# Kernel tuning notes

Hardware: AMD Instinct MI355X
Metric: run time of the kernel (lower is better)

The kernel has to match this reference:

```python
import jax, jax.numpy as jnp
import numpy as np

TEMPERATURE = 0.5
EPS = 1e-12  # matches torch F.normalize default eps


def setup_inputs() -> dict:
    key = jax.random.key(0)
    k1, k2 = jax.random.split(key)
    B, D = 4096, 1024
    emb_i = jax.random.normal(k1, (B, D), dtype=jnp.float32)
    emb_j = jax.random.normal(k2, (B, D), dtype=jnp.float32)
    return {"emb_i": emb_i, "emb_j": emb_j}


def _l2_normalize(x):
    # torch F.normalize(dim=1): x / max(||x||, eps)
    n = jnp.sqrt(jnp.sum(x * x, axis=1, keepdims=True))
    return x / jnp.maximum(n, EPS)


def reference(emb_i, emb_j):
    B = emb_i.shape[0]
    z_i = _l2_normalize(emb_i)
    z_j = _l2_normalize(emb_j)
    z = jnp.concatenate([z_i, z_j], axis=0)  # [2B, D]
    # cosine similarity of unit vectors == dot product -> single GEMM
    sim = jnp.einsum('nd,md->nm', z, z)  # [2B, 2B]
    sim_ij = jnp.diagonal(sim, offset=B)   # [B]
    sim_ji = jnp.diagonal(sim, offset=-B)  # [B]
    positives = jnp.concatenate([sim_ij, sim_ji], axis=0)  # [2B]
    nominator = jnp.exp(positives / TEMPERATURE)
    neg_mask = 1.0 - jnp.eye(2 * B, dtype=sim.dtype)
    denominator = jnp.sum(neg_mask * jnp.exp(sim / TEMPERATURE), axis=1)  # [2B]
    loss_partial = -jnp.log(nominator / denominator)
    return jnp.sum(loss_partial) / (2 * B)
```

## Files before the change

### kernel.cpp

```cpp
#include <hip/hip_runtime.h>
#include <hip/hip_bf16.h>
#include <math.h>

#define B_ROWS 4096
#define N_ROWS 8192
#define D_DIM  1024
#define NTILES 64
#define NSLOT  64
#define NPAIRS (NTILES * (NTILES + 1) / 2)
#define NXCD 8

#define BM 128
#define BK 64
#define NT (D_DIM / BK)
#define SLOT_BYTES 16384
#define RING 2

typedef __attribute__((ext_vector_type(4))) int i32x4;

__device__ __forceinline__ void load_lds_16B(const void* g, void* l) {
  __builtin_amdgcn_global_load_lds(
      (const __attribute__((address_space(1))) void*)g,
      (__attribute__((address_space(3))) void*)l, 16, 0, 0);
}

#define VMCNT0() asm volatile("s_waitcnt vmcnt(0)" ::: "memory")
#define LGKM0()  asm volatile("s_waitcnt lgkmcnt(0)" ::: "memory")
#define BARRIER() asm volatile("s_barrier" ::: "memory")

__global__ __launch_bounds__(256) void normalize_kernel(
    const float* __restrict__ emb_i, const float* __restrict__ emb_j,
    char* __restrict__ zq, float* __restrict__ rowS) {
  const int lane = threadIdx.x & 63;
  const int wave = threadIdx.x >> 6;
  const int row = blockIdx.x * 4 + wave;
  const float* src = (row < B_ROWS) ? (emb_i + (size_t)row * D_DIM)
                                    : (emb_j + (size_t)(row - B_ROWS) * D_DIM);
  const float4* s4 = reinterpret_cast<const float4*>(src);
  float4 v0 = s4[lane], v1 = s4[lane + 64], v2 = s4[lane + 128],
         v3 = s4[lane + 192];

  float ss = v0.x * v0.x + v0.y * v0.y + v0.z * v0.z + v0.w * v0.w +
             v1.x * v1.x + v1.y * v1.y + v1.z * v1.z + v1.w * v1.w +
             v2.x * v2.x + v2.y * v2.y + v2.z * v2.z + v2.w * v2.w +
             v3.x * v3.x + v3.y * v3.y + v3.z * v3.z + v3.w * v3.w;
#pragma unroll
  for (int m = 32; m; m >>= 1) ss += __shfl_xor(ss, m, 64);
  const float scale = 1.0f / fmaxf(sqrtf(ss), 1e-12f);

  float z[16];
  z[0] = v0.x * scale;  z[1] = v0.y * scale;  z[2] = v0.z * scale;
  z[3] = v0.w * scale;  z[4] = v1.x * scale;  z[5] = v1.y * scale;
  z[6] = v1.z * scale;  z[7] = v1.w * scale;  z[8] = v2.x * scale;
  z[9] = v2.y * scale;  z[10] = v2.z * scale; z[11] = v2.w * scale;
  z[12] = v3.x * scale; z[13] = v3.y * scale; z[14] = v3.z * scale;
  z[15] = v3.w * scale;

  float am = 0.0f;
#pragma unroll
  for (int i = 0; i < 16; ++i) am = fmaxf(am, fabsf(z[i]));
#pragma unroll
  for (int m = 32; m; m >>= 1) am = fmaxf(am, __shfl_xor(am, m, 64));
  const float s = am * (1.0f / 127.0f);
  const float inv = (am > 0.0f) ? 127.0f / am : 0.0f;

  char4* dst = reinterpret_cast<char4*>(zq + (size_t)row * D_DIM);
#pragma unroll
  for (int i = 0; i < 4; ++i) {
    char4 pk;
    pk.x = (char)(int)rintf(z[i * 4 + 0] * inv);
    pk.y = (char)(int)rintf(z[i * 4 + 1] * inv);
    pk.z = (char)(int)rintf(z[i * 4 + 2] * inv);
    pk.w = (char)(int)rintf(z[i * 4 + 3] * inv);
    dst[lane + 64 * i] = pk;
  }
  if (lane == 0) rowS[row] = s;
}

__global__ __launch_bounds__(256, 4) void simexp_kernel(
    const char* __restrict__ zq, const float* __restrict__ rowS,
    float* __restrict__ partial, float* __restrict__ dn,
    float* __restrict__ pos) {
  __shared__ __align__(16) char ldsbuf[RING * SLOT_BYTES];
  __shared__ float rowAcc[BM];
  __shared__ float colAcc[BM];
  __shared__ float sRow[BM];
  __shared__ float sCol[BM];

  const int tid = threadIdx.x;

  const int work = (blockIdx.x % NXCD) * (NPAIRS / NXCD) + blockIdx.x / NXCD;

  int rem = work;
  int ti = 0;
  while (rem >= NTILES - ti) {
    rem -= NTILES - ti;
    ++ti;
  }
  const int tj = ti + rem;
  const bool diag = (ti == tj);
  const int row0 = ti * BM;
  const int m0 = tj * BM;

  if (tid < BM) {
    rowAcc[tid] = 0.0f;
    sRow[tid] = rowS[row0 + tid];
  } else {
    colAcc[tid - BM] = 0.0f;
    sCol[tid - BM] = rowS[m0 + tid - BM];
  }

  const int wave = tid >> 6, lane = tid & 63;
  const int wr = wave >> 1, wc = wave & 1;
  const int l15 = lane & 15, l4 = lane >> 4;

  const int rs = tid >> 2;
  const int qs = tid & 3;
  const int ss = qs ^ ((rs >> 1) & 3);
  const char* gA0 = zq + (size_t)(row0 + rs) * D_DIM + ss * 16;
  const size_t dR64 = (size_t)64 * D_DIM;
  const size_t dB = (size_t)(m0 - row0) * D_DIM;
  const int WA0 = tid * 16;
  const int WA1 = tid * 16 + 4096;

  int offA[4], offB[4];
#pragma unroll
  for (int mi = 0; mi < 4; ++mi) {
    const int rA = wr * 64 + mi * 16 + l15;
    offA[mi] = rA * 64 + ((l4 ^ ((rA >> 1) & 3)) << 4);
    const int rB = wc * 64 + mi * 16 + l15;
    offB[mi] = 8192 + rB * 64 + ((l4 ^ ((rB >> 1) & 3)) << 4);
  }

  i32x4 acc[4][4];
#pragma unroll
  for (int mi = 0; mi < 4; ++mi)
#pragma unroll
    for (int ni = 0; ni < 4; ++ni) acc[mi][ni] = (i32x4){0, 0, 0, 0};

#define STAGE(kk)                                                      \
  {                                                                    \
    char* slot_ = ldsbuf + ((kk) & (RING - 1)) * SLOT_BYTES;           \
    const char* g_ = gA0 + (size_t)(kk)*BK;                            \
    load_lds_16B(g_, slot_ + WA0);                                     \
    load_lds_16B(g_ + dR64, slot_ + WA1);                              \
    load_lds_16B(g_ + dB, slot_ + 8192 + WA0);                         \
    load_lds_16B(g_ + dB + dR64, slot_ + 8192 + WA1);                  \
  }

#define COMPUTE(kk)                                                    \
  {                                                                    \
    const char* slot_ = ldsbuf + ((kk) & (RING - 1)) * SLOT_BYTES;     \
    i32x4 af[4], bf[4];                                                \
    _Pragma("unroll") for (int mi = 0; mi < 4; ++mi)                   \
        af[mi] = *reinterpret_cast<const i32x4*>(slot_ + offA[mi]);    \
    _Pragma("unroll") for (int ni = 0; ni < 4; ++ni)                   \
        bf[ni] = *reinterpret_cast<const i32x4*>(slot_ + offB[ni]);    \
    __builtin_amdgcn_s_setprio(1);                                     \
    _Pragma("unroll") for (int mi = 0; mi < 4; ++mi)                   \
        _Pragma("unroll") for (int ni = 0; ni < 4; ++ni) acc[mi][ni] = \
            __builtin_amdgcn_mfma_i32_16x16x64_i8(af[mi], bf[ni],      \
                                                  acc[mi][ni], 0, 0,   \
                                                  0);                  \
    __builtin_amdgcn_s_setprio(0);                                     \
  }

  STAGE(0);
  VMCNT0();
  BARRIER();

  for (int k = 0; k < NT - 1; ++k) {
    STAGE(k + 1);
    COMPUTE(k);
    VMCNT0();
    BARRIER();
  }
  COMPUTE(NT - 1);

  if (diag || tj == ti + 32) {
    float* dst = diag ? dn : pos;
    if (wr == wc) {
#pragma unroll
      for (int mi = 0; mi < 4; ++mi) {
#pragma unroll
        for (int j = 0; j < 4; ++j) {
          if (l15 == l4 * 4 + j) {
            const int rloc = wr * 64 + mi * 16 + l4 * 4 + j;
            dst[row0 + rloc] =
                sRow[rloc] * sCol[rloc] * (float)acc[mi][mi][j];
          }
        }
      }
    }
  }

  const float C2 = 2.8853900817779268f;
  float cCol0 = C2 * sCol[wc * 64 + 0 * 16 + l15];
  float cCol1 = C2 * sCol[wc * 64 + 1 * 16 + l15];
  float cCol2 = C2 * sCol[wc * 64 + 2 * 16 + l15];
  float cCol3 = C2 * sCol[wc * 64 + 3 * 16 + l15];

#pragma unroll
  for (int mi = 0; mi < 4; ++mi) {
#pragma unroll
    for (int j = 0; j < 4; ++j) {
      const float srow = sRow[wr * 64 + mi * 16 + l4 * 4 + j];
      acc[mi][0][j] = __float_as_int(exp2f(cCol0 * srow * (float)acc[mi][0][j]));
      acc[mi][1][j] = __float_as_int(exp2f(cCol1 * srow * (float)acc[mi][1][j]));
      acc[mi][2][j] = __float_as_int(exp2f(cCol2 * srow * (float)acc[mi][2][j]));
      acc[mi][3][j] = __float_as_int(exp2f(cCol3 * srow * (float)acc[mi][3][j]));
    }
  }

#pragma unroll
  for (int mi = 0; mi < 4; ++mi) {
#pragma unroll
    for (int j = 0; j < 4; ++j) {
      float s = __int_as_float(acc[mi][0][j]) + __int_as_float(acc[mi][1][j]) +
                __int_as_float(acc[mi][2][j]) + __int_as_float(acc[mi][3][j]);
      s += __shfl_xor(s, 1, 64);
      s += __shfl_xor(s, 2, 64);
      s += __shfl_xor(s, 4, 64);
      s += __shfl_xor(s, 8, 64);
      if (l15 == 0) atomicAdd(&rowAcc[wr * 64 + mi * 16 + l4 * 4 + j], s);
    }
  }

  if (!diag) {
#pragma unroll
    for (int ni = 0; ni < 4; ++ni) {
      float s = 0.0f;
#pragma unroll
      for (int mi = 0; mi < 4; ++mi)
#pragma unroll
        for (int j = 0; j < 4; ++j) s += __int_as_float(acc[mi][ni][j]);
      s += __shfl_xor(s, 16, 64);
      s += __shfl_xor(s, 32, 64);
      if (l4 == 0) atomicAdd(&colAcc[wc * 64 + ni * 16 + l15], s);
    }
  }

  LGKM0();
  BARRIER();
  if (tid < BM) partial[(size_t)(row0 + tid) * NSLOT + tj] = rowAcc[tid];
  if (!diag && tid >= BM && tid < 2 * BM)
    partial[(size_t)(m0 + tid - BM) * NSLOT + ti] = colAcc[tid - BM];
#undef STAGE
#undef COMPUTE
}

__global__ void rowloss_kernel(const float* __restrict__ partial,
                               const float* __restrict__ dn,
                               const float* __restrict__ pos,
                               float* __restrict__ blockSum) {
  const int tid = threadIdx.x;
  const int n = blockIdx.x * 256 + tid;
  const float C2 = 2.8853900817779268f;
  float S = 0.0f;
#pragma unroll
  for (int c = 0; c < NSLOT; ++c) S += partial[(size_t)n * NSLOT + c];
  const float den = S - exp2f(dn[n] * C2);
  const float p = pos[(n < B_ROWS) ? n : (n - B_ROWS)];
  float acc = -2.0f * p + logf(den);
#pragma unroll
  for (int m = 32; m; m >>= 1) acc += __shfl_xor(acc, m, 64);
  __shared__ float red[4];
  const int wave = tid >> 6, lane = tid & 63;
  if (lane == 0) red[wave] = acc;
  __syncthreads();
  if (tid == 0) blockSum[blockIdx.x] = red[0] + red[1] + red[2] + red[3];
}

__global__ void final2_kernel(const float* __restrict__ blockSum,
                              float* __restrict__ out) {
  const int tid = threadIdx.x;
  float v = (tid < 32) ? blockSum[tid] : 0.0f;
#pragma unroll
  for (int m = 32; m; m >>= 1) v += __shfl_xor(v, m, 64);
  if (tid == 0) out[0] = v / (float)N_ROWS;
}

extern "C" void kernel_launch(void* const* d_in, const int* in_sizes, int n_in,
                              void* d_out, int out_size, void* d_ws,
                              size_t ws_size, hipStream_t stream) {
  const float* emb_i = (const float*)d_in[0];
  const float* emb_j = (const float*)d_in[1];
  float* out = (float*)d_out;

  char* zq = (char*)d_ws;
  char* p = (char*)d_ws + (size_t)N_ROWS * D_DIM;
  float* partial = (float*)p;
  p += (size_t)N_ROWS * NSLOT * sizeof(float);
  float* dn = (float*)p;
  p += (size_t)N_ROWS * sizeof(float);
  float* rowS = (float*)p;
  p += (size_t)N_ROWS * sizeof(float);
  float* pos = (float*)p;
  p += (size_t)B_ROWS * sizeof(float);
  float* blockSum = (float*)p;

  normalize_kernel<<<N_ROWS / 4, 256, 0, stream>>>(emb_i, emb_j, zq, rowS);
  simexp_kernel<<<NPAIRS, 256, 0, stream>>>(zq, rowS, partial, dn, pos);
  rowloss_kernel<<<N_ROWS / 256, 256, 0, stream>>>(partial, dn, pos, blockSum);
  final2_kernel<<<1, 64, 0, stream>>>(blockSum, out);
}
```

Measured before the change: 75.89 us.

## Enlarge similarity tiles to 256x256 with 8-wave ping-pong MFMA schedule

The int8 similarity GEMM tile grows from 128x128 to 256x256, with K-step 128 and 512-thread blocks of 8 waves. This cuts the number of triangular tile pairs from 2080 to 528 and doubles operand reuse per LDS load. The main loop now interleaves global-to-LDS staging of the next double buffer with LDS fragment reads and barrier-separated MFMA bursts, using a new 8-way XOR swizzle. The cost is a 128KB LDS footprint, which likely allows only one block per CU. With only 528 blocks there is also a risk of tail imbalance and many extra barriers.

```diff
diff --git a/kernel.cpp b/kernel.cpp
--- a/kernel.cpp
+++ b/kernel.cpp
@@ -5,16 +5,16 @@
 #define B_ROWS 4096
 #define N_ROWS 8192
 #define D_DIM  1024
-#define NTILES 64
-#define NSLOT  64
+#define NTILES 32
+#define NSLOT  32
 #define NPAIRS (NTILES * (NTILES + 1) / 2)
 #define NXCD 8
-
-#define BM 128
-#define BK 64
+#define POSOFF 16
+
+#define BM 256
+#define BK 128
 #define NT (D_DIM / BK)
-#define SLOT_BYTES 16384
-#define RING 2
+#define BUF_BYTES 65536
 
 typedef __attribute__((ext_vector_type(4))) int i32x4;
 
@@ -77,11 +77,11 @@
   if (lane == 0) rowS[row] = s;
 }
 
-__global__ __launch_bounds__(256, 4) void simexp_kernel(
+__global__ __launch_bounds__(512, 2) void simexp_kernel(
     const char* __restrict__ zq, const float* __restrict__ rowS,
     float* __restrict__ partial, float* __restrict__ dn,
     float* __restrict__ pos) {
-  __shared__ __align__(16) char ldsbuf[RING * SLOT_BYTES];
+  __shared__ __align__(16) char ldsbuf[2 * BUF_BYTES];
   __shared__ float rowAcc[BM];
   __shared__ float colAcc[BM];
   __shared__ float sRow[BM];
@@ -111,109 +111,140 @@
   }
 
   const int wave = tid >> 6, lane = tid & 63;
-  const int wr = wave >> 1, wc = wave & 1;
+  const int wr = wave >> 2, wc = wave & 3;
   const int l15 = lane & 15, l4 = lane >> 4;
 
-  const int rs = tid >> 2;
-  const int qs = tid & 3;
-  const int ss = qs ^ ((rs >> 1) & 3);
-  const char* gA0 = zq + (size_t)(row0 + rs) * D_DIM + ss * 16;
-  const size_t dR64 = (size_t)64 * D_DIM;
+  const int lr = tid >> 3;
+  const int sp = tid & 7;
+  const int sl = sp ^ (lr & 7);
+  const char* gA = zq + (size_t)(row0 + lr) * D_DIM + sl * 16;
   const size_t dB = (size_t)(m0 - row0) * D_DIM;
-  const int WA0 = tid * 16;
-  const int WA1 = tid * 16 + 4096;
-
-  int offA[4], offB[4];
-#pragma unroll
-  for (int mi = 0; mi < 4; ++mi) {
-    const int rA = wr * 64 + mi * 16 + l15;
-    offA[mi] = rA * 64 + ((l4 ^ ((rA >> 1) & 3)) << 4);
-    const int rB = wc * 64 + mi * 16 + l15;
-    offB[mi] = 8192 + rB * 64 + ((l4 ^ ((rB >> 1) & 3)) << 4);
-  }
-
-  i32x4 acc[4][4];
-#pragma unroll
-  for (int mi = 0; mi < 4; ++mi)
+  const int WD = tid * 16;
+
+  const int xk0 = ((l4 ^ (l15 & 7)) << 4);
+  const int xk1 = (((4 + l4) ^ (l15 & 7)) << 4);
+
+  i32x4 acc[8][4];
+#pragma unroll
+  for (int mi = 0; mi < 8; ++mi)
 #pragma unroll
     for (int ni = 0; ni < 4; ++ni) acc[mi][ni] = (i32x4){0, 0, 0, 0};
 
-#define STAGE(kk)                                                      \
+#define STAGE_ROUND(kk, rr)                                                  \
+  load_lds_16B(gA + ((rr) < 4 ? (size_t)0 : dB) + (size_t)((rr)&3) * 65536 + \
+                   (size_t)(kk)*BK,                                          \
+               ldsbuf + ((kk)&1) * BUF_BYTES + ((rr) < 4 ? 0 : 32768) +      \
+                   ((rr)&3) * 8192 + WD)
+
+#define RD_A(mh, ks)                                                   \
   {                                                                    \
-    char* slot_ = ldsbuf + ((kk) & (RING - 1)) * SLOT_BYTES;           \
-    const char* g_ = gA0 + (size_t)(kk)*BK;                            \
-    load_lds_16B(g_, slot_ + WA0);                                     \
-    load_lds_16B(g_ + dR64, slot_ + WA1);                              \
-    load_lds_16B(g_ + dB, slot_ + 8192 + WA0);                         \
-    load_lds_16B(g_ + dB + dR64, slot_ + 8192 + WA1);                  \
-  }
-
-#define COMPUTE(kk)                                                    \
+    const char* ba_ = slot + (wr * 128 + (mh)*64) * 128;               \
+    const int xo_ = (ks) ? xk1 : xk0;                                  \
+    af0 = *reinterpret_cast<const i32x4*>(ba_ + (l15) * 128 + xo_);    \
+    af1 = *reinterpret_cast<const i32x4*>(ba_ + (l15 + 16) * 128 + xo_); \
+    af2 = *reinterpret_cast<const i32x4*>(ba_ + (l15 + 32) * 128 + xo_); \
+    af3 = *reinterpret_cast<const i32x4*>(ba_ + (l15 + 48) * 128 + xo_); \
+  }
+
+#define RD_B(nh, ks)                                                   \
   {                                                                    \
-    const char* slot_ = ldsbuf + ((kk) & (RING - 1)) * SLOT_BYTES;     \
-    i32x4 af[4], bf[4];                                                \
-    _Pragma("unroll") for (int mi = 0; mi < 4; ++mi)                   \
-        af[mi] = *reinterpret_cast<const i32x4*>(slot_ + offA[mi]);    \
-    _Pragma("unroll") for (int ni = 0; ni < 4; ++ni)                   \
-        bf[ni] = *reinterpret_cast<const i32x4*>(slot_ + offB[ni]);    \
-    __builtin_amdgcn_s_setprio(1);                                     \
-    _Pragma("unroll") for (int mi = 0; mi < 4; ++mi)                   \
-        _Pragma("unroll") for (int ni = 0; ni < 4; ++ni) acc[mi][ni] = \
-            __builtin_amdgcn_mfma_i32_16x16x64_i8(af[mi], bf[ni],      \
-                                                  acc[mi][ni], 0, 0,   \
-                                                  0);                  \
-    __builtin_amdgcn_s_setprio(0);                                     \
-  }
-
-  STAGE(0);
+    const char* bb_ = slot + 32768 + (wc * 64 + (nh)*32) * 128;        \
+    const int xo_ = (ks) ? xk1 : xk0;                                  \
+    bf0 = *reinterpret_cast<const i32x4*>(bb_ + (l15) * 128 + xo_);    \
+    bf1 = *reinterpret_cast<const i32x4*>(bb_ + (l15 + 16) * 128 + xo_); \
+  }
+
+#define MFMA8(mh, nh)                                                      \
+  __builtin_amdgcn_s_setprio(1);                                           \
+  acc[(mh)*4 + 0][(nh)*2 + 0] = __builtin_amdgcn_mfma_i32_16x16x64_i8(     \
+      af0, bf0, acc[(mh)*4 + 0][(nh)*2 + 0], 0, 0, 0);                     \
+  acc[(mh)*4 + 1][(nh)*2 + 0] = __builtin_amdgcn_mfma_i32_16x16x64_i8(     \
+      af1, bf0, acc[(mh)*4 + 1][(nh)*2 + 0], 0, 0, 0);                     \
+  acc[(mh)*4 + 2][(nh)*2 + 0] = __builtin_amdgcn_mfma_i32_16x16x64_i8(     \
+      af2, bf0, acc[(mh)*4 + 2][(nh)*2 + 0], 0, 0, 0);                     \
+  acc[(mh)*4 + 3][(nh)*2 + 0] = __builtin_amdgcn_mfma_i32_16x16x64_i8(     \
+      af3, bf0, acc[(mh)*4 + 3][(nh)*2 + 0], 0, 0, 0);                     \
+  acc[(mh)*4 + 0][(nh)*2 + 1] = __builtin_amdgcn_mfma_i32_16x16x64_i8(     \
+      af0, bf1, acc[(mh)*4 + 0][(nh)*2 + 1], 0, 0, 0);                     \
+  acc[(mh)*4 + 1][(nh)*2 + 1] = __builtin_amdgcn_mfma_i32_16x16x64_i8(     \
+      af1, bf1, acc[(mh)*4 + 1][(nh)*2 + 1], 0, 0, 0);                     \
+  acc[(mh)*4 + 2][(nh)*2 + 1] = __builtin_amdgcn_mfma_i32_16x16x64_i8(     \
+      af2, bf1, acc[(mh)*4 + 2][(nh)*2 + 1], 0, 0, 0);                     \
+  acc[(mh)*4 + 3][(nh)*2 + 1] = __builtin_amdgcn_mfma_i32_16x16x64_i8(     \
+      af3, bf1, acc[(mh)*4 + 3][(nh)*2 + 1], 0, 0, 0);                     \
+  __builtin_amdgcn_s_setprio(0);
+
+  STAGE_ROUND(0, 0); STAGE_ROUND(0, 1); STAGE_ROUND(0, 2); STAGE_ROUND(0, 3);
+  STAGE_ROUND(0, 4); STAGE_ROUND(0, 5); STAGE_ROUND(0, 6); STAGE_ROUND(0, 7);
   VMCNT0();
   BARRIER();
 
-  for (int k = 0; k < NT - 1; ++k) {
-    STAGE(k + 1);
-    COMPUTE(k);
+  for (int k = 0; k < NT; ++k) {
+    const char* slot = ldsbuf + (k & 1) * BUF_BYTES;
+    const bool st = (k < NT - 1);
+    i32x4 af0, af1, af2, af3, bf0, bf1;
+
+    RD_A(0, 0); RD_B(0, 0);
+    if (st) { STAGE_ROUND(k + 1, 0); STAGE_ROUND(k + 1, 1); }
+    BARRIER(); MFMA8(0, 0); BARRIER();
+    RD_B(1, 0);
+    if (st) { STAGE_ROUND(k + 1, 2); STAGE_ROUND(k + 1, 3); }
+    BARRIER(); MFMA8(0, 1); BARRIER();
+    RD_A(1, 0); RD_B(0, 0);
+    if (st) { STAGE_ROUND(k + 1, 4); STAGE_ROUND(k + 1, 5); }
+    BARRIER(); MFMA8(1, 0); BARRIER();
+    RD_B(1, 0);
+    if (st) { STAGE_ROUND(k + 1, 6); STAGE_ROUND(k + 1, 7); }
+    BARRIER(); MFMA8(1, 1); BARRIER();
+    RD_A(0, 1); RD_B(0, 1);
+    BARRIER(); MFMA8(0, 0); BARRIER();
+    RD_B(1, 1);
+    BARRIER(); MFMA8(0, 1); BARRIER();
+    RD_A(1, 1); RD_B(0, 1);
+    BARRIER(); MFMA8(1, 0); BARRIER();
+    RD_B(1, 1);
+    BARRIER(); MFMA8(1, 1);
     VMCNT0();
     BARRIER();
   }
-  COMPUTE(NT - 1);
-
-  if (diag || tj == ti + 32) {
+
+  if (diag || tj == ti + POSOFF) {
     float* dst = diag ? dn : pos;
-    if (wr == wc) {
-#pragma unroll
-      for (int mi = 0; mi < 4; ++mi) {
+#pragma unroll
+    for (int mi = 0; mi < 8; ++mi) {
+#pragma unroll
+      for (int ni = 0; ni < 4; ++ni) {
 #pragma unroll
         for (int j = 0; j < 4; ++j) {
-          if (l15 == l4 * 4 + j) {
-            const int rloc = wr * 64 + mi * 16 + l4 * 4 + j;
-            dst[row0 + rloc] =
-                sRow[rloc] * sCol[rloc] * (float)acc[mi][mi][j];
-          }
+          const int rl = wr * 128 + mi * 16 + l4 * 4 + j;
+          const int cl = wc * 64 + ni * 16 + l15;
+          if (rl == cl)
+            dst[row0 + rl] = sRow[rl] * sCol[cl] * (float)acc[mi][ni][j];
         }
       }
     }
   }
 
   const float C2 = 2.8853900817779268f;
-  float cCol0 = C2 * sCol[wc * 64 + 0 * 16 + l15];
-  float cCol1 = C2 * sCol[wc * 64 + 1 * 16 + l15];
-  float cCol2 = C2 * sCol[wc * 64 + 2 * 16 + l15];
-  float cCol3 = C2 * sCol[wc * 64 + 3 * 16 + l15];
-
-#pragma unroll
-  for (int mi = 0; mi < 4; ++mi) {
+  const float cc0 = C2 * sCol[wc * 64 + 0 * 16 + l15];
+  const float cc1 = C2 * sCol[wc * 64 + 1 * 16 + l15];
+  const float cc2 = C2 * sCol[wc * 64 + 2 * 16 + l15];
+  const float cc3 = C2 * sCol[wc * 64 + 3 * 16 + l15];
+
+#pragma unroll
+  for (int mi = 0; mi < 8; ++mi) {
 #pragma unroll
     for (int j = 0; j < 4; ++j) {
-      const float srow = sRow[wr * 64 + mi * 16 + l4 * 4 + j];
-      acc[mi][0][j] = __float_as_int(exp2f(cCol0 * srow * (float)acc[mi][0][j]));
-      acc[mi][1][j] = __float_as_int(exp2f(cCol1 * srow * (float)acc[mi][1][j]));
-      acc[mi][2][j] = __float_as_int(exp2f(cCol2 * srow * (float)acc[mi][2][j]));
-      acc[mi][3][j] = __float_as_int(exp2f(cCol3 * srow * (float)acc[mi][3][j]));
+      const float srow = sRow[wr * 128 + mi * 16 + l4 * 4 + j];
+      acc[mi][0][j] = __float_as_int(exp2f(cc0 * srow * (float)acc[mi][0][j]));
+      acc[mi][1][j] = __float_as_int(exp2f(cc1 * srow * (float)acc[mi][1][j]));
+      acc[mi][2][j] = __float_as_int(exp2f(cc2 * srow * (float)acc[mi][2][j]));
+      acc[mi][3][j] = __float_as_int(exp2f(cc3 * srow * (float)acc[mi][3][j]));
     }
   }
 
 #pragma unroll
-  for (int mi = 0; mi < 4; ++mi) {
+  for (int mi = 0; mi < 8; ++mi) {
 #pragma unroll
     for (int j = 0; j < 4; ++j) {
       float s = __int_as_float(acc[mi][0][j]) + __int_as_float(acc[mi][1][j]) +
@@ -222,7 +253,7 @@
       s += __shfl_xor(s, 2, 64);
       s += __shfl_xor(s, 4, 64);
       s += __shfl_xor(s, 8, 64);
-      if (l15 == 0) atomicAdd(&rowAcc[wr * 64 + mi * 16 + l4 * 4 + j], s);
+      if (l15 == 0) atomicAdd(&rowAcc[wr * 128 + mi * 16 + l4 * 4 + j], s);
     }
   }
 
@@ -231,7 +262,7 @@
     for (int ni = 0; ni < 4; ++ni) {
       float s = 0.0f;
 #pragma unroll
-      for (int mi = 0; mi < 4; ++mi)
+      for (int mi = 0; mi < 8; ++mi)
 #pragma unroll
         for (int j = 0; j < 4; ++j) s += __int_as_float(acc[mi][ni][j]);
       s += __shfl_xor(s, 16, 64);
@@ -245,8 +276,10 @@
   if (tid < BM) partial[(size_t)(row0 + tid) * NSLOT + tj] = rowAcc[tid];
   if (!diag && tid >= BM && tid < 2 * BM)
     partial[(size_t)(m0 + tid - BM) * NSLOT + ti] = colAcc[tid - BM];
-#undef STAGE
-#undef COMPUTE
+#undef STAGE_ROUND
+#undef RD_A
+#undef RD_B
+#undef MFMA8
 }
 
 __global__ void rowloss_kernel(const float* __restrict__ partial,
@@ -300,7 +333,7 @@
   float* blockSum = (float*)p;
 
   normalize_kernel<<<N_ROWS / 4, 256, 0, stream>>>(emb_i, emb_j, zq, rowS);
-  simexp_kernel<<<NPAIRS, 256, 0, stream>>>(zq, rowS, partial, dn, pos);
+  simexp_kernel<<<NPAIRS, 512, 0, stream>>>(zq, rowS, partial, dn, pos);
   rowloss_kernel<<<N_ROWS / 256, 256, 0, stream>>>(partial, dn, pos, blockSum);
   final2_kernel<<<1, 64, 0, stream>>>(blockSum, out);
 }
```

After: 92.66 us. +22.1%, slower.
